# Optimization experiments

Measured on AMD Instinct MI355X. Metric: run time of the kernel, lower is better.

Reference implementation:

```python
import jax, jax.numpy as jnp
import numpy as np

D_MODEL = 1024
N_HEADS = 16
D_HEAD = D_MODEL // N_HEADS
D_FF = 4096
B, T = 2, 2048


def setup_inputs() -> dict:
    key = jax.random.key(0)
    ks = jax.random.split(key, 8)
    s = 0.02
    return {
        "x": jax.random.normal(ks[0], (B, T, D_MODEL), dtype=jnp.float32),
        "wq": jax.random.normal(ks[1], (D_MODEL, D_MODEL), dtype=jnp.float32) * s,
        "wk": jax.random.normal(ks[2], (D_MODEL, D_MODEL), dtype=jnp.float32) * s,
        "wv": jax.random.normal(ks[3], (D_MODEL, D_MODEL), dtype=jnp.float32) * s,
        "wo": jax.random.normal(ks[4], (D_MODEL, D_MODEL), dtype=jnp.float32) * s,
        "w1": jax.random.normal(ks[5], (D_FF, D_MODEL), dtype=jnp.float32) * s,
        "b1": jnp.zeros((D_FF,), dtype=jnp.float32),
        "w2": jax.random.normal(ks[6], (D_MODEL, D_FF), dtype=jnp.float32) * s,
        "b2": jnp.zeros((D_MODEL,), dtype=jnp.float32),
        "ln1_g": jnp.ones((D_MODEL,), dtype=jnp.float32),
        "ln1_b": jnp.zeros((D_MODEL,), dtype=jnp.float32),
        "ln2_g": jnp.ones((D_MODEL,), dtype=jnp.float32),
        "ln2_b": jnp.zeros((D_MODEL,), dtype=jnp.float32),
    }


def _layernorm(x, g, b, eps=1e-5):
    mu = jnp.mean(x, axis=-1, keepdims=True)
    var = jnp.mean(jnp.square(x - mu), axis=-1, keepdims=True)
    return (x - mu) * jax.lax.rsqrt(var + eps) * g + b


def reference(x, wq, wk, wv, wo, w1, b1, w2, b2, ln1_g, ln1_b, ln2_g, ln2_b):
    Bsz, Tlen, C = x.shape
    h = _layernorm(x, ln1_g, ln1_b)
    # torch Linear: y = h @ W^T ; reshape to [B, H, T, Dh]
    def proj(w):
        return (h @ w.T).reshape(Bsz, Tlen, N_HEADS, D_HEAD).transpose(0, 2, 1, 3)
    q, k, v = proj(wq), proj(wk), proj(wv)
    scores = jnp.einsum('bhqd,bhkd->bhqk', q, k) / np.sqrt(D_HEAD).astype(np.float32)
    p = jax.nn.softmax(scores.astype(jnp.float32), axis=-1).astype(scores.dtype)
    out = jnp.einsum('bhqk,bhkd->bhqd', p, v)
    out = out.transpose(0, 2, 1, 3).reshape(Bsz, Tlen, C)
    x = x + out @ wo.T
    h2 = _layernorm(x, ln2_g, ln2_b)
    ff = jax.nn.gelu(h2 @ w1.T + b1, approximate=False) @ w2.T + b2
    return x + ff
```

## Files before the change

kernel.cpp:

```cpp
#include <hip/hip_runtime.h>
#include <hip/hip_bf16.h>
#include <math.h>

#define DM   1024
#define NH   16
#define DH   64
#define DFF  4096
#define BB   2
#define TT   2048
#define MTOK (BB*TT)
#define QS   3072

typedef unsigned short u16;
typedef unsigned int   u32;
typedef __attribute__((ext_vector_type(8))) __bf16 bf16x8;
typedef __attribute__((ext_vector_type(4))) float  f32x4;

__device__ inline float bf2f(u16 u) { return __uint_as_float(((u32)u) << 16); }
__device__ inline u16 f2bf(float f) {
  u32 u = __float_as_uint(f);
  u += 0x7FFFu + ((u >> 16) & 1u);
  return (u16)(u >> 16);
}
__device__ inline u32 packtrunc(float lo, float hi) {
  return __builtin_amdgcn_perm(__float_as_uint(hi), __float_as_uint(lo), 0x07060302u);
}
__device__ inline float fexp2(float x) { return __builtin_amdgcn_exp2f(x); }

__device__ inline void gload_lds16(const void* g, void* l) {
  __builtin_amdgcn_global_load_lds(
      (const __attribute__((address_space(1))) void*)g,
      (__attribute__((address_space(3))) void*)l,
      16, 0, 0);
}

__global__ __launch_bounds__(256) void prep(
    const float* __restrict__ wq, const float* __restrict__ wk, const float* __restrict__ wv,
    const float* __restrict__ wo, const float* __restrict__ w1, const float* __restrict__ w2,
    const float* __restrict__ x, const float* __restrict__ g, const float* __restrict__ be,
    u16* __restrict__ wqkv_b, u16* __restrict__ wo_b, u16* __restrict__ w1_b,
    u16* __restrict__ w2_b, u16* __restrict__ h1)
{
  const int blk = blockIdx.x;
  if (blk < 12288) {
    const float* src; u16* dst; int idx;
    if (blk < 3072) {
      idx = blk * 256 + threadIdx.x;
      const int sel = idx >> 18;
      const int j = idx & 0x3FFFF;
      src = sel == 0 ? wq : (sel == 1 ? wk : wv);
      dst = wqkv_b;
      float4 v = ((const float4*)src)[j];
      ushort4 o; o.x = f2bf(v.x); o.y = f2bf(v.y); o.z = f2bf(v.z); o.w = f2bf(v.w);
      ((ushort4*)dst)[idx] = o;
      return;
    } else if (blk < 4096) { src = wo; dst = wo_b; idx = (blk - 3072) * 256 + threadIdx.x; }
    else if (blk < 8192)   { src = w1; dst = w1_b; idx = (blk - 4096) * 256 + threadIdx.x; }
    else                   { src = w2; dst = w2_b; idx = (blk - 8192) * 256 + threadIdx.x; }
    float4 v = ((const float4*)src)[idx];
    ushort4 o; o.x = f2bf(v.x); o.y = f2bf(v.y); o.z = f2bf(v.z); o.w = f2bf(v.w);
    ((ushort4*)dst)[idx] = o;
    return;
  }
  const int w = threadIdx.x >> 6, lane = threadIdx.x & 63;
  const int row = (blk - 12288) * 4 + w;
  const float4* xr = (const float4*)(x + (size_t)row * DM);
  float4 v[4];
  float s = 0.f, s2 = 0.f;
#pragma unroll
  for (int i = 0; i < 4; i++) {
    v[i] = xr[i * 64 + lane];
    s  += v[i].x + v[i].y + v[i].z + v[i].w;
    s2 += v[i].x * v[i].x + v[i].y * v[i].y + v[i].z * v[i].z + v[i].w * v[i].w;
  }
#pragma unroll
  for (int off = 32; off > 0; off >>= 1) {
    s  += __shfl_xor(s,  off);
    s2 += __shfl_xor(s2, off);
  }
  const float mu = s * (1.f / DM);
  const float rs = rsqrtf(s2 * (1.f / DM) - mu * mu + 1e-5f);
  u16* orow = h1 + (size_t)row * DM;
#pragma unroll
  for (int i = 0; i < 4; i++) {
    const float4 gg = ((const float4*)g)[i * 64 + lane];
    const float4 bb = ((const float4*)be)[i * 64 + lane];
    ushort4 o;
    o.x = f2bf((v[i].x - mu) * rs * gg.x + bb.x);
    o.y = f2bf((v[i].y - mu) * rs * gg.y + bb.y);
    o.z = f2bf((v[i].z - mu) * rs * gg.z + bb.z);
    o.w = f2bf((v[i].w - mu) * rs * gg.w + bb.w);
    ((ushort4*)orow)[i * 64 + lane] = o;
  }
}

__global__ __launch_bounds__(256) void reduce_ln(
    const float* __restrict__ x, const float* __restrict__ P,
    const float* __restrict__ g, const float* __restrict__ be,
    float* __restrict__ xmid, u16* __restrict__ h2)
{
  const float* P0 = P;
  const float* P1 = P + (size_t)MTOK * DM;
  const int w = threadIdx.x >> 6, lane = threadIdx.x & 63;
  const int row = blockIdx.x * 4 + w;
  const size_t roff = (size_t)row * DM;
  float4 v[4];
  float s = 0.f, s2 = 0.f;
#pragma unroll
  for (int i = 0; i < 4; i++) {
    const float4 a = ((const float4*)(x  + roff))[i * 64 + lane];
    const float4 p = ((const float4*)(P0 + roff))[i * 64 + lane];
    const float4 qv = ((const float4*)(P1 + roff))[i * 64 + lane];
    v[i].x = a.x + p.x + qv.x; v[i].y = a.y + p.y + qv.y;
    v[i].z = a.z + p.z + qv.z; v[i].w = a.w + p.w + qv.w;
    ((float4*)(xmid + roff))[i * 64 + lane] = v[i];
    s  += v[i].x + v[i].y + v[i].z + v[i].w;
    s2 += v[i].x * v[i].x + v[i].y * v[i].y + v[i].z * v[i].z + v[i].w * v[i].w;
  }
#pragma unroll
  for (int off = 32; off > 0; off >>= 1) {
    s  += __shfl_xor(s,  off);
    s2 += __shfl_xor(s2, off);
  }
  const float mu = s * (1.f / DM);
  const float rs = rsqrtf(s2 * (1.f / DM) - mu * mu + 1e-5f);
  u16* orow = h2 + roff;
#pragma unroll
  for (int i = 0; i < 4; i++) {
    const float4 gg = ((const float4*)g)[i * 64 + lane];
    const float4 bb = ((const float4*)be)[i * 64 + lane];
    ushort4 o;
    o.x = f2bf((v[i].x - mu) * rs * gg.x + bb.x);
    o.y = f2bf((v[i].y - mu) * rs * gg.y + bb.y);
    o.z = f2bf((v[i].z - mu) * rs * gg.z + bb.z);
    o.w = f2bf((v[i].w - mu) * rs * gg.w + bb.w);
    ((ushort4*)orow)[i * 64 + lane] = o;
  }
}

__global__ __launch_bounds__(256) void reduce_out(
    const float* __restrict__ Q, const float* __restrict__ xmid,
    const float* __restrict__ b2, float* __restrict__ out)
{
  const float* Q0 = Q;
  const float* Q1 = Q + (size_t)MTOK * DM;
  const int i = blockIdx.x * 256 + threadIdx.x;
  const float4 a = ((const float4*)xmid)[i];
  const float4 p = ((const float4*)Q0)[i];
  const float4 qv = ((const float4*)Q1)[i];
  const float4 bb = ((const float4*)b2)[i & (DM / 4 - 1)];
  float4 o;
  o.x = a.x + p.x + qv.x + bb.x; o.y = a.y + p.y + qv.y + bb.y;
  o.z = a.z + p.z + qv.z + bb.z; o.w = a.w + p.w + qv.w + bb.w;
  ((float4*)out)[i] = o;
}

template <int EPI, int BN>
__global__ __launch_bounds__(256) void gemm_bt(
    const u16* __restrict__ A, const u16* __restrict__ Bw,
    int M, int N, int K,
    const float* __restrict__ bias,
    u16* __restrict__ outB, float oscale, int scaleN)
{
  constexpr int NJ = BN / 32;
  __shared__ u16 As[128 * 64];
  __shared__ u16 Bs[BN * 64];

  const int tid  = threadIdx.x;
  const int w    = tid >> 6;
  const int lane = tid & 63;
  const int wr   = w >> 1, wc = w & 1;
  const int q    = lane >> 4;
  const int li   = lane & 15;
  const int rowBase = blockIdx.y * 128;
  const int colBase = blockIdx.x * BN;

  const int lr = lane >> 3;
  const int cs = (lane & 7) ^ lr;
  const u16* Abase = A  + (size_t)(rowBase + lr) * K + cs * 8;
  const u16* Bbase = Bw + (size_t)(colBase + lr) * K + cs * 8;

  f32x4 acc[4][NJ] = {};

  for (int k0 = 0; k0 < K; k0 += 64) {
    __syncthreads();
#pragma unroll
    for (int jj = 0; jj < 4; jj++) {
      const int rb = (w * 4 + jj) * 8;
      gload_lds16(Abase + (size_t)rb * K + k0, &As[rb * 64]);
    }
#pragma unroll
    for (int jj = 0; jj < NJ; jj++) {
      const int rb = (w * NJ + jj) * 8;
      gload_lds16(Bbase + (size_t)rb * K + k0, &Bs[rb * 64]);
    }
    __syncthreads();
#pragma unroll
    for (int kk = 0; kk < 2; kk++) {
      bf16x8 fa[4], fb[NJ];
      const int pos = (kk * 4 + q) ^ (li & 7);
#pragma unroll
      for (int i = 0; i < 4; i++) {
        const int row = wr * 64 + i * 16 + li;
        fa[i] = *(const bf16x8*)&As[row * 64 + pos * 8];
      }
#pragma unroll
      for (int j = 0; j < NJ; j++) {
        const int row = wc * (BN / 2) + j * 16 + li;
        fb[j] = *(const bf16x8*)&Bs[row * 64 + pos * 8];
      }
#pragma unroll
      for (int i = 0; i < 4; i++)
#pragma unroll
        for (int j = 0; j < NJ; j++)
          acc[i][j] = __builtin_amdgcn_mfma_f32_16x16x32_bf16(fa[i], fb[j], acc[i][j], 0, 0, 0);
    }
  }

#pragma unroll
  for (int i = 0; i < 4; i++) {
#pragma unroll
    for (int j = 0; j < NJ; j++) {
      const int col = colBase + wc * (BN / 2) + j * 16 + li;
      float bv = 0.f;
      if constexpr (EPI == 2) bv = bias[col];
#pragma unroll
      for (int r = 0; r < 4; r++) {
        const int row = rowBase + wr * 64 + i * 16 + q * 4 + r;
        float v = acc[i][j][r] + bv;
        if constexpr (EPI == 2) {
          const float z = fexp2(-v * (2.302213f + 0.1029625f * v * v));
          v = v * __builtin_amdgcn_rcpf(1.f + z);
        }
        if constexpr (EPI == 0) {
          const float sc = (col < scaleN) ? oscale : 1.f;
          v *= sc;
        }
        outB[(size_t)row * N + col] = f2bf(v);
      }
    }
  }
}

template <int EPI, int KC>
__global__ __launch_bounds__(512, 2) void gemm256(
    const u16* __restrict__ A, const u16* __restrict__ Bw,
    int N,
    const float* __restrict__ bias,
    u16* __restrict__ outB, float oscale, int scaleN)
{
  constexpr int K  = KC;
  constexpr int NT = KC / 32;
  __shared__ u16 lds[4 * 16384];

  const int tid  = threadIdx.x;
  const int w    = tid >> 6;
  const int lane = tid & 63;
  const int wr   = w >> 2, wc = w & 3;
  const int q    = lane >> 4, li = lane & 15;

  const int nbx = gridDim.x;
  const int o   = blockIdx.y * nbx + blockIdx.x;
  const int xcd = o & 7, i_x = o >> 3;
  const int nsx = nbx >> 2;
  const int super = xcd + 8 * (i_x >> 4);
  const int wi  = i_x & 15;
  const int bx  = (super % nsx) * 4 + (wi & 3);
  const int by  = (super / nsx) * 4 + (wi >> 2);
  const int rowBase = by * 256, colBase = bx * 256;

  const int srow = lane >> 2;
  const int schk = (lane & 3) ^ ((lane >> 3) & 3);
  const u16* Asrc = A  + (size_t)(rowBase + srow) * K + schk * 8;
  const u16* Bsrc = Bw + (size_t)(colBase + srow) * K + schk * 8;

  auto stageA = [&](int kt, int bsel) {
    const int k0 = kt * 32;
    u16* dst = &lds[bsel * 16384];
#pragma unroll
    for (int j = 0; j < 2; j++) {
      const int rb = w * 32 + j * 16;
      gload_lds16(Asrc + (size_t)rb * K + k0, &dst[rb * 32]);
    }
  };
  auto stageB = [&](int kt, int bsel) {
    const int k0 = kt * 32;
    u16* dst = &lds[bsel * 16384 + 8192];
#pragma unroll
    for (int j = 0; j < 2; j++) {
      const int rb = w * 32 + j * 16;
      gload_lds16(Bsrc + (size_t)rb * K + k0, &dst[rb * 32]);
    }
  };

  f32x4 acc[8][4] = {};
  const int pos = q ^ ((li >> 1) & 3);

  stageA(0, 0); stageB(0, 0);
  stageA(1, 1); stageB(1, 1);
  stageA(2, 2); stageB(2, 2);

  for (int t = 0; t < NT; ++t) {
    if (t < NT - 2)      asm volatile("s_waitcnt vmcnt(8)" ::: "memory");
    else if (t == NT - 2) asm volatile("s_waitcnt vmcnt(4)" ::: "memory");
    else                 asm volatile("s_waitcnt vmcnt(0)" ::: "memory");
    __builtin_amdgcn_s_barrier();

    const u16* bb = &lds[(t & 3) * 16384];
    bf16x8 fa[4], fb[4];

#pragma unroll
    for (int m = 0; m < 4; m++)
      fa[m] = *(const bf16x8*)&bb[(wr * 128 + m * 16 + li) * 32 + pos * 8];
#pragma unroll
    for (int n = 0; n < 4; n++)
      fb[n] = *(const bf16x8*)&bb[8192 + (wc * 64 + n * 16 + li) * 32 + pos * 8];
    if (t + 3 < NT) stageA(t + 3, (t + 3) & 3);
    __builtin_amdgcn_s_barrier();
    __builtin_amdgcn_s_setprio(1);
#pragma unroll
    for (int m = 0; m < 4; m++)
#pragma unroll
      for (int n = 0; n < 4; n++)
        acc[m][n] = __builtin_amdgcn_mfma_f32_16x16x32_bf16(fa[m], fb[n], acc[m][n], 0, 0, 0);
    __builtin_amdgcn_s_setprio(0);
    __builtin_amdgcn_s_barrier();

#pragma unroll
    for (int m = 0; m < 4; m++)
      fa[m] = *(const bf16x8*)&bb[(wr * 128 + 64 + m * 16 + li) * 32 + pos * 8];
    if (t + 3 < NT) stageB(t + 3, (t + 3) & 3);
    __builtin_amdgcn_s_barrier();
    __builtin_amdgcn_s_setprio(1);
#pragma unroll
    for (int m = 0; m < 4; m++)
#pragma unroll
      for (int n = 0; n < 4; n++)
        acc[4 + m][n] = __builtin_amdgcn_mfma_f32_16x16x32_bf16(fa[m], fb[n], acc[4 + m][n], 0, 0, 0);
    __builtin_amdgcn_s_setprio(0);
  }

#pragma unroll
  for (int n = 0; n < 4; n++) {
    const int col = colBase + wc * 64 + n * 16 + li;
    float bv = 0.f;
    if constexpr (EPI == 2) bv = bias[col];
#pragma unroll
    for (int m = 0; m < 8; m++) {
#pragma unroll
      for (int r = 0; r < 4; r++) {
        const int row = rowBase + wr * 128 + m * 16 + q * 4 + r;
        float v = acc[m][n][r] + bv;
        if constexpr (EPI == 2) {
          const float z = fexp2(-v * (2.302213f + 0.1029625f * v * v));
          v = v * __builtin_amdgcn_rcpf(1.f + z);
        }
        if constexpr (EPI == 0) {
          const float sc = (col < scaleN) ? oscale : 1.f;
          v *= sc;
        }
        outB[(size_t)row * N + col] = f2bf(v);
      }
    }
  }
}

__global__ __launch_bounds__(256) void gemm_sk(
    const u16* __restrict__ A, const u16* __restrict__ Bw,
    int N, int K, int KLEN, float* __restrict__ P)
{
  __shared__ u16 As[128 * 64];
  __shared__ u16 Bs[64 * 64];

  const int tid  = threadIdx.x;
  const int w    = tid >> 6;
  const int lane = tid & 63;
  const int wr   = w >> 1, wc = w & 1;
  const int q    = lane >> 4;
  const int li   = lane & 15;
  const int rowBase = blockIdx.y * 128;
  const int colBase = blockIdx.x * 64;
  const int koff = blockIdx.z * KLEN;

  const int lr = lane >> 3;
  const int cs = (lane & 7) ^ lr;
  const u16* Abase = A  + (size_t)(rowBase + lr) * K + koff + cs * 8;
  const u16* Bbase = Bw + (size_t)(colBase + lr) * K + koff + cs * 8;

  f32x4 acc[4][2] = {};

  for (int k0 = 0; k0 < KLEN; k0 += 64) {
    __syncthreads();
#pragma unroll
    for (int jj = 0; jj < 4; jj++) {
      const int rb = (w * 4 + jj) * 8;
      gload_lds16(Abase + (size_t)rb * K + k0, &As[rb * 64]);
    }
#pragma unroll
    for (int jj = 0; jj < 2; jj++) {
      const int rb = (w * 2 + jj) * 8;
      gload_lds16(Bbase + (size_t)rb * K + k0, &Bs[rb * 64]);
    }
    __syncthreads();
#pragma unroll
    for (int kk = 0; kk < 2; kk++) {
      bf16x8 fa[4], fb[2];
      const int pos = (kk * 4 + q) ^ (li & 7);
#pragma unroll
      for (int i = 0; i < 4; i++) {
        const int row = wr * 64 + i * 16 + li;
        fa[i] = *(const bf16x8*)&As[row * 64 + pos * 8];
      }
#pragma unroll
      for (int j = 0; j < 2; j++) {
        const int row = wc * 32 + j * 16 + li;
        fb[j] = *(const bf16x8*)&Bs[row * 64 + pos * 8];
      }
#pragma unroll
      for (int i = 0; i < 4; i++)
#pragma unroll
        for (int j = 0; j < 2; j++)
          acc[i][j] = __builtin_amdgcn_mfma_f32_16x16x32_bf16(fa[i], fb[j], acc[i][j], 0, 0, 0);
    }
  }

  float* Pz = P + (size_t)blockIdx.z * MTOK * DM;
#pragma unroll
  for (int i = 0; i < 4; i++)
#pragma unroll
    for (int j = 0; j < 2; j++) {
      const int col = colBase + wc * 32 + j * 16 + li;
#pragma unroll
      for (int r = 0; r < 4; r++) {
        const int row = rowBase + wr * 64 + i * 16 + q * 4 + r;
        Pz[(size_t)row * N + col] = acc[i][j][r];
      }
    }
}

__global__ __launch_bounds__(256) void transpose_v(
    const u16* __restrict__ vq, u16* __restrict__ vt)
{
  __shared__ u16 t[64][72];
  const int bh = blockIdx.x, b = bh >> 4, h = bh & 15;
  const int t0 = blockIdx.y * 64;
  const int tid = threadIdx.x;
  const int r = tid >> 2, c = (tid & 3) * 16;
  const u16* src = vq + (size_t)(b * TT + t0 + r) * QS + h * DH + c;
#pragma unroll
  for (int i = 0; i < 4; i++)
    *(ushort4*)&t[r][c + i * 4] = ((const ushort4*)src)[i];
  __syncthreads();
  const int dh = tid >> 2, tt = (tid & 3) * 16;
  u16* dst = vt + ((size_t)bh * 64 + dh) * TT + t0 + tt;
#pragma unroll
  for (int i = 0; i < 4; i++) {
    ushort4 o;
    o.x = t[tt + i * 4 + 0][dh]; o.y = t[tt + i * 4 + 1][dh];
    o.z = t[tt + i * 4 + 2][dh]; o.w = t[tt + i * 4 + 3][dh];
    ((ushort4*)dst)[i] = o;
  }
}

__global__ __launch_bounds__(512) void attn_mfma(
    const u16* __restrict__ qb, const u16* __restrict__ kb,
    const u16* __restrict__ vt, u16* __restrict__ ob)
{
  __shared__ u16 Ks[2][64 * 64];
  __shared__ u16 Vs[2][64 * 64];
  __shared__ u16 Sh[8 * 16 * 72];

  const int tid = threadIdx.x, w = tid >> 6, lane = tid & 63;
  const int q = lane >> 4, li = lane & 15;
  const int bh = blockIdx.x, b = bh >> 4, h = bh & 15;
  const int q0 = blockIdx.y * 128;
  const int lr8 = lane >> 3, lc8 = lane & 7;

#pragma unroll
  for (int jj = 0; jj < 2; jj++) {
    const int rb = w * 16 + jj * 8;
    const int row = rb + lr8;
    const int cs = lc8 ^ (row & 7);
    gload_lds16(qb + (size_t)(b * TT + q0 + row) * QS + h * DH + cs * 8,
                &Sh[rb * 64]);
  }
  __syncthreads();

  bf16x8 qf[2];
#pragma unroll
  for (int kk = 0; kk < 2; kk++) {
    const int row = w * 16 + li;
    const int pos = (kk * 4 + q) ^ (li & 7);
    qf[kk] = *(const bf16x8*)&Sh[row * 64 + pos * 8];
  }

  auto stage = [&](int buf, int kt) {
    const int rb = w * 8;
    const int row = rb + lr8;
    const int cs = lc8 ^ (row & 7);
    gload_lds16(kb + (size_t)(b * TT + kt + row) * QS + h * DH + cs * 8,
                &Ks[buf][rb * 64]);
    gload_lds16(vt + ((size_t)bh * 64 + row) * TT + kt + cs * 8,
                &Vs[buf][rb * 64]);
  };

  f32x4 ot[4] = {};
  float lsum = 0.f;
  u16* Pw = &Sh[w * 16 * 72];

  stage(0, 0);
  for (int it = 0; it < TT / 64; it++) {
    __syncthreads();
    if (it + 1 < TT / 64) stage((it + 1) & 1, (it + 1) * 64);
    const u16* Kc = Ks[it & 1];
    const u16* Vc = Vs[it & 1];

    f32x4 st[4] = {};
#pragma unroll
    for (int kk = 0; kk < 2; kk++)
#pragma unroll
      for (int i = 0; i < 4; i++) {
        const int pos = (kk * 4 + q) ^ (li & 7);
        const bf16x8 kf = *(const bf16x8*)&Kc[(i * 16 + li) * 64 + pos * 8];
        st[i] = __builtin_amdgcn_mfma_f32_16x16x32_bf16(kf, qf[kk], st[i], 0, 0, 0);
      }

    u32 pk[4][2];
#pragma unroll
    for (int i = 0; i < 4; i++) {
      const float p0 = fexp2(st[i][0]);
      const float p1 = fexp2(st[i][1]);
      const float p2 = fexp2(st[i][2]);
      const float p3 = fexp2(st[i][3]);
      lsum += (p0 + p1) + (p2 + p3);
      pk[i][0] = packtrunc(p0, p1);
      pk[i][1] = packtrunc(p2, p3);
    }

#pragma unroll
    for (int i = 0; i < 4; i++) {
      const int a = li * 72 + i * 16 + q * 4;
      *(u32*)&Pw[a]     = pk[i][0];
      *(u32*)&Pw[a + 2] = pk[i][1];
    }

#pragma unroll
    for (int kk = 0; kk < 2; kk++) {
      const bf16x8 pf = *(const bf16x8*)&Pw[li * 72 + kk * 32 + q * 8];
#pragma unroll
      for (int m = 0; m < 4; m++) {
        const int pos = (kk * 4 + q) ^ (li & 7);
        const bf16x8 vf = *(const bf16x8*)&Vc[(m * 16 + li) * 64 + pos * 8];
        ot[m] = __builtin_amdgcn_mfma_f32_16x16x32_bf16(vf, pf, ot[m], 0, 0, 0);
      }
    }
  }

  float s = lsum;
  s += __shfl_xor(s, 16);
  s += __shfl_xor(s, 32);
  const float inv = 1.f / s;
#pragma unroll
  for (int m = 0; m < 4; m++) {
    const int a = li * 72 + m * 16 + q * 4;
    *(u32*)&Pw[a]     = packtrunc(ot[m][0] * inv, ot[m][1] * inv);
    *(u32*)&Pw[a + 2] = packtrunc(ot[m][2] * inv, ot[m][3] * inv);
  }
#pragma unroll
  for (int pass = 0; pass < 2; pass++) {
    const int row = pass * 8 + lr8;
    const bf16x8 v = *(const bf16x8*)&Pw[row * 72 + lc8 * 8];
    const int token = q0 + w * 16 + row;
    *(bf16x8*)(ob + ((size_t)(b * TT + token) * NH + h) * DH + lc8 * 8) = v;
  }
}

extern "C" void kernel_launch(void* const* d_in, const int* in_sizes, int n_in,
                              void* d_out, int out_size, void* d_ws, size_t ws_size,
                              hipStream_t stream) {
  const float* x    = (const float*)d_in[0];
  const float* wq   = (const float*)d_in[1];
  const float* wk   = (const float*)d_in[2];
  const float* wv   = (const float*)d_in[3];
  const float* wo   = (const float*)d_in[4];
  const float* w1   = (const float*)d_in[5];
  const float* b1   = (const float*)d_in[6];
  const float* w2   = (const float*)d_in[7];
  const float* b2   = (const float*)d_in[8];
  const float* ln1g = (const float*)d_in[9];
  const float* ln1b = (const float*)d_in[10];
  const float* ln2g = (const float*)d_in[11];
  const float* ln2b = (const float*)d_in[12];

  size_t off = 0;
  char* base = (char*)d_ws;
  auto alloc = [&](size_t bytes) { void* p = base + off; off += bytes; return p; };

  u16* wqkv_b = (u16*)alloc((size_t)3 * DM * DM * 2);
  u16* wo_b   = (u16*)alloc((size_t)DM * DM * 2);
  u16* w1_b   = (u16*)alloc((size_t)DFF * DM * 2);
  u16* w2_b   = (u16*)alloc((size_t)DM * DFF * 2);
  u16* h1     = (u16*)alloc((size_t)MTOK * DM * 2);
  u16* qkvb   = (u16*)alloc((size_t)MTOK * QS * 2);
  u16* attn   = (u16*)alloc((size_t)MTOK * DM * 2);
  u16* h2     = (u16*)alloc((size_t)MTOK * DM * 2);
  u16* ff1    = (u16*)alloc((size_t)MTOK * DFF * 2);
  float* xmid = (float*)alloc((size_t)MTOK * DM * 4);
  u16* vtb    = ff1;
  float* woP  = (float*)ff1;
  float* ff2P = (float*)h1;
  (void)ws_size; (void)in_sizes; (void)n_in; (void)out_size;

  prep<<<13312, 256, 0, stream>>>(wq, wk, wv, wo, w1, w2, x, ln1g, ln1b,
                                  wqkv_b, wo_b, w1_b, w2_b, h1);

  const float QSCALE = 0.125f * 1.44269504088896340736f;
  gemm_bt<0, 128><<<dim3(QS / 128, MTOK / 128), 256, 0, stream>>>(
      h1, wqkv_b, MTOK, QS, DM, nullptr, qkvb, QSCALE, DM);

  transpose_v<<<dim3(BB * NH, TT / 64), 256, 0, stream>>>(qkvb + 2 * DM, vtb);
  attn_mfma<<<dim3(BB * NH, TT / 128), 512, 0, stream>>>(qkvb, qkvb + DM, vtb, attn);

  gemm_sk<<<dim3(DM / 64, MTOK / 128, 2), 256, 0, stream>>>(
      attn, wo_b, DM, DM, DM / 2, woP);
  reduce_ln<<<MTOK / 4, 256, 0, stream>>>(x, woP, ln2g, ln2b, xmid, h2);

  gemm256<2, DM><<<dim3(DFF / 256, MTOK / 256), 512, 0, stream>>>(
      h2, w1_b, DFF, b1, ff1, 1.f, 0);
  gemm_sk<<<dim3(DM / 64, MTOK / 128, 2), 256, 0, stream>>>(
      ff1, w2_b, DM, DFF, DFF / 2, ff2P);
  reduce_out<<<MTOK * DM / 4 / 256, 256, 0, stream>>>(ff2P, xmid, b2, (float*)d_out);
}
```

Baseline: 335.2 us.

## Replace split-K partials with full-K GEMMs fusing residual and bias epilogues

```diff
diff --git a/kernel.cpp b/kernel.cpp
--- a/kernel.cpp
+++ b/kernel.cpp
@@ -13,6 +13,7 @@
 
 typedef unsigned short u16;
 typedef unsigned int   u32;
+typedef unsigned long long u64;
 typedef __attribute__((ext_vector_type(8))) __bf16 bf16x8;
 typedef __attribute__((ext_vector_type(4))) float  f32x4;
 
@@ -94,13 +95,10 @@
   }
 }
 
-__global__ __launch_bounds__(256) void reduce_ln(
-    const float* __restrict__ x, const float* __restrict__ P,
-    const float* __restrict__ g, const float* __restrict__ be,
-    float* __restrict__ xmid, u16* __restrict__ h2)
+__global__ __launch_bounds__(256) void ln2k(
+    const float* __restrict__ xm, const float* __restrict__ g,
+    const float* __restrict__ be, u16* __restrict__ h2)
 {
-  const float* P0 = P;
-  const float* P1 = P + (size_t)MTOK * DM;
   const int w = threadIdx.x >> 6, lane = threadIdx.x & 63;
   const int row = blockIdx.x * 4 + w;
   const size_t roff = (size_t)row * DM;
@@ -108,12 +106,7 @@
   float s = 0.f, s2 = 0.f;
 #pragma unroll
   for (int i = 0; i < 4; i++) {
-    const float4 a = ((const float4*)(x  + roff))[i * 64 + lane];
-    const float4 p = ((const float4*)(P0 + roff))[i * 64 + lane];
-    const float4 qv = ((const float4*)(P1 + roff))[i * 64 + lane];
-    v[i].x = a.x + p.x + qv.x; v[i].y = a.y + p.y + qv.y;
-    v[i].z = a.z + p.z + qv.z; v[i].w = a.w + p.w + qv.w;
-    ((float4*)(xmid + roff))[i * 64 + lane] = v[i];
+    v[i] = ((const float4*)(xm + roff))[i * 64 + lane];
     s  += v[i].x + v[i].y + v[i].z + v[i].w;
     s2 += v[i].x * v[i].x + v[i].y * v[i].y + v[i].z * v[i].z + v[i].w * v[i].w;
   }
@@ -136,23 +129,6 @@
     o.w = f2bf((v[i].w - mu) * rs * gg.w + bb.w);
     ((ushort4*)orow)[i * 64 + lane] = o;
   }
-}
-
-__global__ __launch_bounds__(256) void reduce_out(
-    const float* __restrict__ Q, const float* __restrict__ xmid,
-    const float* __restrict__ b2, float* __restrict__ out)
-{
-  const float* Q0 = Q;
-  const float* Q1 = Q + (size_t)MTOK * DM;
-  const int i = blockIdx.x * 256 + threadIdx.x;
-  const float4 a = ((const float4*)xmid)[i];
-  const float4 p = ((const float4*)Q0)[i];
-  const float4 qv = ((const float4*)Q1)[i];
-  const float4 bb = ((const float4*)b2)[i & (DM / 4 - 1)];
-  float4 o;
-  o.x = a.x + p.x + qv.x + bb.x; o.y = a.y + p.y + qv.y + bb.y;
-  o.z = a.z + p.z + qv.z + bb.z; o.w = a.w + p.w + qv.w + bb.w;
-  ((float4*)out)[i] = o;
 }
 
 template <int EPI, int BN>
@@ -242,6 +218,87 @@
   }
 }
 
+template <int EPI>
+__global__ __launch_bounds__(256) void gemm_f32out(
+    const u16* __restrict__ A, const u16* __restrict__ Bw,
+    int N, int K,
+    const float* __restrict__ res, const float* __restrict__ bias,
+    float* __restrict__ out)
+{
+  __shared__ u16 As[128 * 64];
+  __shared__ u16 Bs[64 * 64];
+
+  const int tid  = threadIdx.x;
+  const int w    = tid >> 6;
+  const int lane = tid & 63;
+  const int wr   = w >> 1, wc = w & 1;
+  const int q    = lane >> 4;
+  const int li   = lane & 15;
+
+  const int nbx = gridDim.x, nwg = nbx * gridDim.y;
+  int o = blockIdx.y * nbx + blockIdx.x;
+  o = (o & 7) * (nwg >> 3) + (o >> 3);
+  const int rowBase = (o / nbx) * 128;
+  const int colBase = (o % nbx) * 64;
+
+  const int lr = lane >> 3;
+  const int cs = (lane & 7) ^ lr;
+  const u16* Abase = A  + (size_t)(rowBase + lr) * K + cs * 8;
+  const u16* Bbase = Bw + (size_t)(colBase + lr) * K + cs * 8;
+
+  f32x4 acc[4][2] = {};
+
+  for (int k0 = 0; k0 < K; k0 += 64) {
+    __syncthreads();
+#pragma unroll
+    for (int jj = 0; jj < 4; jj++) {
+      const int rb = (w * 4 + jj) * 8;
+      gload_lds16(Abase + (size_t)rb * K + k0, &As[rb * 64]);
+    }
+#pragma unroll
+    for (int jj = 0; jj < 2; jj++) {
+      const int rb = (w * 2 + jj) * 8;
+      gload_lds16(Bbase + (size_t)rb * K + k0, &Bs[rb * 64]);
+    }
+    __syncthreads();
+#pragma unroll
+    for (int kk = 0; kk < 2; kk++) {
+      bf16x8 fa[4], fb[2];
+      const int pos = (kk * 4 + q) ^ (li & 7);
+#pragma unroll
+      for (int i = 0; i < 4; i++) {
+        const int row = wr * 64 + i * 16 + li;
+        fa[i] = *(const bf16x8*)&As[row * 64 + pos * 8];
+      }
+#pragma unroll
+      for (int j = 0; j < 2; j++) {
+        const int row = wc * 32 + j * 16 + li;
+        fb[j] = *(const bf16x8*)&Bs[row * 64 + pos * 8];
+      }
+#pragma unroll
+      for (int i = 0; i < 4; i++)
+#pragma unroll
+        for (int j = 0; j < 2; j++)
+          acc[i][j] = __builtin_amdgcn_mfma_f32_16x16x32_bf16(fa[i], fb[j], acc[i][j], 0, 0, 0);
+    }
+  }
+
+#pragma unroll
+  for (int i = 0; i < 4; i++)
+#pragma unroll
+    for (int j = 0; j < 2; j++) {
+      const int col = colBase + wc * 32 + j * 16 + li;
+      float bv = 0.f;
+      if constexpr (EPI == 4) bv = bias[col];
+#pragma unroll
+      for (int r = 0; r < 4; r++) {
+        const int row = rowBase + wr * 64 + i * 16 + q * 4 + r;
+        out[(size_t)row * N + col] =
+            acc[i][j][r] + res[(size_t)row * N + col] + bv;
+      }
+    }
+}
+
 template <int EPI, int KC>
 __global__ __launch_bounds__(512, 2) void gemm256(
     const u16* __restrict__ A, const u16* __restrict__ Bw,
@@ -365,79 +422,6 @@
   }
 }
 
-__global__ __launch_bounds__(256) void gemm_sk(
-    const u16* __restrict__ A, const u16* __restrict__ Bw,
-    int N, int K, int KLEN, float* __restrict__ P)
-{
-  __shared__ u16 As[128 * 64];
-  __shared__ u16 Bs[64 * 64];
-
-  const int tid  = threadIdx.x;
-  const int w    = tid >> 6;
-  const int lane = tid & 63;
-  const int wr   = w >> 1, wc = w & 1;
-  const int q    = lane >> 4;
-  const int li   = lane & 15;
-  const int rowBase = blockIdx.y * 128;
-  const int colBase = blockIdx.x * 64;
-  const int koff = blockIdx.z * KLEN;
-
-  const int lr = lane >> 3;
-  const int cs = (lane & 7) ^ lr;
-  const u16* Abase = A  + (size_t)(rowBase + lr) * K + koff + cs * 8;
-  const u16* Bbase = Bw + (size_t)(colBase + lr) * K + koff + cs * 8;
-
-  f32x4 acc[4][2] = {};
-
-  for (int k0 = 0; k0 < KLEN; k0 += 64) {
-    __syncthreads();
-#pragma unroll
-    for (int jj = 0; jj < 4; jj++) {
-      const int rb = (w * 4 + jj) * 8;
-      gload_lds16(Abase + (size_t)rb * K + k0, &As[rb * 64]);
-    }
-#pragma unroll
-    for (int jj = 0; jj < 2; jj++) {
-      const int rb = (w * 2 + jj) * 8;
-      gload_lds16(Bbase + (size_t)rb * K + k0, &Bs[rb * 64]);
-    }
-    __syncthreads();
-#pragma unroll
-    for (int kk = 0; kk < 2; kk++) {
-      bf16x8 fa[4], fb[2];
-      const int pos = (kk * 4 + q) ^ (li & 7);
-#pragma unroll
-      for (int i = 0; i < 4; i++) {
-        const int row = wr * 64 + i * 16 + li;
-        fa[i] = *(const bf16x8*)&As[row * 64 + pos * 8];
-      }
-#pragma unroll
-      for (int j = 0; j < 2; j++) {
-        const int row = wc * 32 + j * 16 + li;
-        fb[j] = *(const bf16x8*)&Bs[row * 64 + pos * 8];
-      }
-#pragma unroll
-      for (int i = 0; i < 4; i++)
-#pragma unroll
-        for (int j = 0; j < 2; j++)
-          acc[i][j] = __builtin_amdgcn_mfma_f32_16x16x32_bf16(fa[i], fb[j], acc[i][j], 0, 0, 0);
-    }
-  }
-
-  float* Pz = P + (size_t)blockIdx.z * MTOK * DM;
-#pragma unroll
-  for (int i = 0; i < 4; i++)
-#pragma unroll
-    for (int j = 0; j < 2; j++) {
-      const int col = colBase + wc * 32 + j * 16 + li;
-#pragma unroll
-      for (int r = 0; r < 4; r++) {
-        const int row = rowBase + wr * 64 + i * 16 + q * 4 + r;
-        Pz[(size_t)row * N + col] = acc[i][j][r];
-      }
-    }
-}
-
 __global__ __launch_bounds__(256) void transpose_v(
     const u16* __restrict__ vq, u16* __restrict__ vt)
 {
@@ -525,7 +509,7 @@
         st[i] = __builtin_amdgcn_mfma_f32_16x16x32_bf16(kf, qf[kk], st[i], 0, 0, 0);
       }
 
-    u32 pk[4][2];
+    u64 pk[4];
 #pragma unroll
     for (int i = 0; i < 4; i++) {
       const float p0 = fexp2(st[i][0]);
@@ -533,16 +517,12 @@
       const float p2 = fexp2(st[i][2]);
       const float p3 = fexp2(st[i][3]);
       lsum += (p0 + p1) + (p2 + p3);
-      pk[i][0] = packtrunc(p0, p1);
-      pk[i][1] = packtrunc(p2, p3);
-    }
-
-#pragma unroll
-    for (int i = 0; i < 4; i++) {
-      const int a = li * 72 + i * 16 + q * 4;
-      *(u32*)&Pw[a]     = pk[i][0];
-      *(u32*)&Pw[a + 2] = pk[i][1];
-    }
+      pk[i] = ((u64)packtrunc(p2, p3) << 32) | packtrunc(p0, p1);
+    }
+
+#pragma unroll
+    for (int i = 0; i < 4; i++)
+      *(u64*)&Pw[li * 72 + i * 16 + q * 4] = pk[i];
 
 #pragma unroll
     for (int kk = 0; kk < 2; kk++) {
@@ -562,9 +542,9 @@
   const float inv = 1.f / s;
 #pragma unroll
   for (int m = 0; m < 4; m++) {
-    const int a = li * 72 + m * 16 + q * 4;
-    *(u32*)&Pw[a]     = packtrunc(ot[m][0] * inv, ot[m][1] * inv);
-    *(u32*)&Pw[a + 2] = packtrunc(ot[m][2] * inv, ot[m][3] * inv);
+    const u64 pv = ((u64)packtrunc(ot[m][2] * inv, ot[m][3] * inv) << 32)
+                 | packtrunc(ot[m][0] * inv, ot[m][1] * inv);
+    *(u64*)&Pw[li * 72 + m * 16 + q * 4] = pv;
   }
 #pragma unroll
   for (int pass = 0; pass < 2; pass++) {
@@ -607,8 +587,6 @@
   u16* ff1    = (u16*)alloc((size_t)MTOK * DFF * 2);
   float* xmid = (float*)alloc((size_t)MTOK * DM * 4);
   u16* vtb    = ff1;
-  float* woP  = (float*)ff1;
-  float* ff2P = (float*)h1;
   (void)ws_size; (void)in_sizes; (void)n_in; (void)out_size;
 
   prep<<<13312, 256, 0, stream>>>(wq, wk, wv, wo, w1, w2, x, ln1g, ln1b,
@@ -621,13 +599,12 @@
   transpose_v<<<dim3(BB * NH, TT / 64), 256, 0, stream>>>(qkvb + 2 * DM, vtb);
   attn_mfma<<<dim3(BB * NH, TT / 128), 512, 0, stream>>>(qkvb, qkvb + DM, vtb, attn);
 
-  gemm_sk<<<dim3(DM / 64, MTOK / 128, 2), 256, 0, stream>>>(
-      attn, wo_b, DM, DM, DM / 2, woP);
-  reduce_ln<<<MTOK / 4, 256, 0, stream>>>(x, woP, ln2g, ln2b, xmid, h2);
+  gemm_f32out<3><<<dim3(DM / 64, MTOK / 128), 256, 0, stream>>>(
+      attn, wo_b, DM, DM, x, nullptr, xmid);
+  ln2k<<<MTOK / 4, 256, 0, stream>>>(xmid, ln2g, ln2b, h2);
 
   gemm256<2, DM><<<dim3(DFF / 256, MTOK / 256), 512, 0, stream>>>(
       h2, w1_b, DFF, b1, ff1, 1.f, 0);
-  gemm_sk<<<dim3(DM / 64, MTOK / 128, 2), 256, 0, stream>>>(
-      ff1, w2_b, DM, DFF, DFF / 2, ff2P);
-  reduce_out<<<MTOK * DM / 4 / 256, 256, 0, stream>>>(ff2P, xmid, b2, (float*)d_out);
-}
+  gemm_f32out<4><<<dim3(DM / 64, MTOK / 128), 256, 0, stream>>>(
+      ff1, w2_b, DM, DFF, xmid, b2, (float*)d_out);
+}
```

After: 330.3 us. Within noise of the previous version (-1.4%).
